# Kernel optimization log

Measured on AMD Instinct MI355X. Metric: run time of the kernel, lower is better.

The kernel has to match this reference:

```python
import jax, jax.numpy as jnp
import numpy as np
import math

B, N, M = 4, 512, 64
F, Q, H, R = 256, 16, 8, 32
D = F // H
ETA = 4.0
EPS = 1e-5
FFN_H = 512

def layer_norm(x, g, b):
    mu = jnp.mean(x, axis=-1, keepdims=True)
    var = jnp.mean((x - mu) ** 2, axis=-1, keepdims=True)
    return (x - mu) * jax.lax.rsqrt(var + EPS) * g + b

def setup_inputs() -> dict:
    key = jax.random.key(0)
    ks = jax.random.split(key, 24)
    def xav(k, shape):
        fan_in, fan_out = shape[1], shape[0]
        std = math.sqrt(2.0 / (fan_in + fan_out))
        return jax.random.normal(k, shape, dtype=jnp.float32) * std
    inp = {
        'a': jax.random.normal(ks[0], (B, N, F), dtype=jnp.float32),
        'charges': jax.random.normal(ks[1], (B, N, Q), dtype=jnp.float32),
        'idx_j': jax.random.randint(ks[2], (B, N, M), 0, N),
        'd_ij': jax.random.uniform(ks[3], (B, N, M), dtype=jnp.float32) * 5.0,
        'mask_ij': jax.random.bernoulli(ks[4], 0.3, (B, N, M)),
        'radial_shifts': jnp.linspace(0.5, 5.0, R, dtype=jnp.float32),
        'Wq': xav(ks[5], (F, F + Q)), 'bq': jnp.zeros((F,), jnp.float32),
        'Wk': xav(ks[6], (F, F + Q)), 'bk': jnp.zeros((F,), jnp.float32),
        'Wv': xav(ks[7], (F, F + Q)), 'bv': jnp.zeros((F,), jnp.float32),
        'Wrb': xav(ks[8], (H, R)), 'brb': jnp.zeros((H,), jnp.float32),
        'Wout': xav(ks[9], (F, 2 * F + R)), 'bout': jnp.zeros((F,), jnp.float32),
        'g1': jnp.ones((F,), jnp.float32), 'b1': jnp.zeros((F,), jnp.float32),
        'g2': jnp.ones((F,), jnp.float32), 'b2': jnp.zeros((F,), jnp.float32),
        'Wf1': xav(ks[10], (FFN_H, F)), 'bf1': jnp.zeros((FFN_H,), jnp.float32),
        'Wf2': xav(ks[11], (F, FFN_H)), 'bf2': jnp.zeros((F,), jnp.float32),
    }
    return inp

def reference(a, charges, idx_j, d_ij, mask_ij, radial_shifts,
              Wq, bq, Wk, bk, Wv, bv, Wrb, brb, Wout, bout,
              g1, b1, g2, b2, Wf1, bf1, Wf2, bf2):
    bidx = jnp.arange(B)[:, None, None]
    a_j = a[bidx, idx_j]          # [B,N,M,F]
    q_j = charges[bidx, idx_j]    # [B,N,M,Q]
    center = jnp.concatenate([a, charges], axis=-1)       # [B,N,F+Q]
    neigh = jnp.concatenate([a_j, q_j], axis=-1)          # [B,N,M,F+Q]
    q = (center @ Wq.T + bq).reshape(B, N, H, D)
    k = (neigh @ Wk.T + bk).reshape(B, N, M, H, D)
    v = (neigh @ Wv.T + bv).reshape(B, N, M, H, D)
    # radial basis: exp(-eta*(d - shift)^2)  -> [B,N,M,R]
    radial = jnp.exp(-ETA * (d_ij[..., None] - radial_shifts) ** 2)
    scores = jnp.einsum('bnhd,bnmhd->bnmh', q, k) / math.sqrt(D)
    scores = scores + radial @ Wrb.T + brb                # [B,N,M,H]
    scores = jnp.swapaxes(scores, -1, -2)                 # [B,N,H,M]
    scores = jnp.where(mask_ij[:, :, None, :], -jnp.inf, scores)
    attn = jax.nn.softmax(scores, axis=-1)
    attn = jnp.nan_to_num(attn, nan=0.0, posinf=0.0, neginf=0.0)
    context = jnp.einsum('bnhm,bnmhd->bnhd', attn, v).reshape(B, N, F)
    radial_context = jnp.einsum('bnhm,bnmg->bnhg', attn, radial).mean(axis=-2)  # [B,N,R]
    update = jnp.concatenate([a, context, radial_context], axis=-1) @ Wout.T + bout
    x = layer_norm(a + update, g1, b1)
    ff = jax.nn.gelu(x @ Wf1.T + bf1, approximate=False) @ Wf2.T + bf2
    return layer_norm(x + ff, g2, b2)
```

## Files before the change

kernel.cpp:

```cpp
#include <hip/hip_runtime.h>
#include <hip/hip_bf16.h>
#include <math.h>

#define Bb 4
#define Nn 512
#define Mm 64
#define Ff 256
#define Qq 16
#define Hh 8
#define Rr 32
#define FFNH 512
#define ROWS (Bb*Nn)
#define KIN (Ff+Qq)
#define KINP 288
#define KOUT (2*Ff+Rr)

typedef short short8 __attribute__((ext_vector_type(8)));
typedef unsigned short ushort8 __attribute__((ext_vector_type(8)));
typedef float f32x4 __attribute__((ext_vector_type(4)));

__device__ inline unsigned short f2b(float f) {
    union { float f; unsigned u; } c; c.f = f;
    unsigned r = c.u + 0x7fffu + ((c.u >> 16) & 1u);
    return (unsigned short)(r >> 16);
}
__device__ inline float b2f(unsigned short u) {
    union { unsigned u; float f; } c; c.u = ((unsigned)u) << 16;
    return c.f;
}

#define OFF_CENTER 0
#define OFF_WQKV   (OFF_CENTER + ROWS*KINP)
#define OFF_WOUT   (OFF_WQKV + 768*KINP)
#define OFF_WF1    (OFF_WOUT + Ff*KOUT)
#define OFF_WF2    (OFF_WF1 + FFNH*Ff)
#define OFF_U      (OFF_WF2 + Ff*FFNH)
#define OFF_XB     (OFF_U + ROWS*KOUT)
#define OFF_FFH    (OFF_XB + ROWS*Ff)
#define OFF_QKVB   (OFF_FFH + ROWS*FFNH)
#define CONV_TOTAL OFF_U
#define CONV_BLK   (CONV_TOTAL/256)
#define A2U_BLK    (ROWS*Ff/256)
#define MSK_BLK    (Bb*Nn*Mm/256)

__global__ __launch_bounds__(256) void prep(const float* __restrict__ a,
                                            const float* __restrict__ ch,
                                            const float* __restrict__ Wq,
                                            const float* __restrict__ Wk,
                                            const float* __restrict__ Wv,
                                            const float* __restrict__ Wout,
                                            const float* __restrict__ Wf1,
                                            const float* __restrict__ Wf2,
                                            const unsigned char* __restrict__ mask,
                                            int* __restrict__ flag,
                                            unsigned short* __restrict__ arena) {
    int bid = blockIdx.x, tid = threadIdx.x;
    if (bid < CONV_BLK) {
        int i = bid * 256 + tid;
        float v;
        if (i < OFF_WQKV) {
            int row = i / KINP, c = i - row * KINP;
            v = (c < Ff) ? a[(size_t)row * Ff + c] : (c < KIN ? ch[(size_t)row * Qq + (c - Ff)] : 0.f);
        } else if (i < OFF_WOUT) {
            int j = i - OFF_WQKV;
            int n = j / KINP, c = j - n * KINP;
            const float* W = n < 256 ? Wq : (n < 512 ? Wk : Wv);
            int nr = n & 255;
            v = (c < KIN) ? W[(size_t)nr * KIN + c] : 0.f;
        } else if (i < OFF_WF1) {
            v = Wout[i - OFF_WOUT];
        } else if (i < OFF_WF2) {
            v = Wf1[i - OFF_WF1];
        } else {
            v = Wf2[i - OFF_WF2];
        }
        arena[i] = f2b(v);
    } else if (bid < CONV_BLK + A2U_BLK) {
        int j = (bid - CONV_BLK) * 256 + tid;
        int row = j >> 8, col = j & 255;
        arena[OFF_U + (size_t)row * KOUT + col] = f2b(a[j]);
    } else {
        int i = (bid - CONV_BLK - A2U_BLK) * 256 + tid;
        if ((i & 3) && mask[i]) *flag = 1;
    }
}

template<int KT, int SPLIT, int MODE>
__global__ __launch_bounds__(256) void gemm_mfma(const unsigned short* __restrict__ Ab, int lda,
                                                 const unsigned short* __restrict__ Wb, int ldw,
                                                 const float* __restrict__ b0,
                                                 const float* __restrict__ b1,
                                                 const float* __restrict__ b2,
                                                 float* __restrict__ C,
                                                 unsigned short* __restrict__ Cb,
                                                 int ldc, size_t pstride) {
    __shared__ unsigned short As[2][64][32];
    __shared__ unsigned short Bs[2][64][32];
    int tid = threadIdx.x;
    int colbase = blockIdx.x * 64;
    int rowbase = blockIdx.y * 64;
    constexpr int TPER = (KT + SPLIT - 1) / SPLIT;
    int t0 = blockIdx.z * TPER;
    int NL = KT - t0; if (NL > TPER) NL = TPER;

    int sr = tid >> 2, sl = tid & 3;
    const unsigned short* Ap = Ab + (size_t)(rowbase + sr) * lda + sl * 8;
    const unsigned short* Wp = Wb + (size_t)(colbase + sr) * ldw + sl * 8;
    int ssw = (sl ^ (sr & 3)) * 8;

    int wave = tid >> 6, lane = tid & 63;
    int wr = (wave >> 1) * 32, wc = (wave & 1) * 32;
    int lrow = lane & 15;
    int kslot = lane >> 4;
    int sp = (kslot ^ (lane & 3)) * 8;

    uint4 av, wv;
    auto prefetch = [&](int t) {
        av = *reinterpret_cast<const uint4*>(Ap + (size_t)t * 32);
        wv = *reinterpret_cast<const uint4*>(Wp + (size_t)t * 32);
    };
    auto writeLDS = [&](int buf) {
        *reinterpret_cast<uint4*>(&As[buf][sr][ssw]) = av;
        *reinterpret_cast<uint4*>(&Bs[buf][sr][ssw]) = wv;
    };

    f32x4 acc[2][2] = {};
    prefetch(t0);
    writeLDS(0);
    __syncthreads();
    for (int tt = 0; tt < NL; ++tt) {
        if (tt + 1 < NL) prefetch(t0 + tt + 1);
        int buf = tt & 1;
        short8 a0 = *reinterpret_cast<const short8*>(&As[buf][wr + lrow][sp]);
        short8 a1 = *reinterpret_cast<const short8*>(&As[buf][wr + 16 + lrow][sp]);
        short8 bv0 = *reinterpret_cast<const short8*>(&Bs[buf][wc + lrow][sp]);
        short8 bv1 = *reinterpret_cast<const short8*>(&Bs[buf][wc + 16 + lrow][sp]);
        acc[0][0] = __builtin_amdgcn_mfma_f32_16x16x32_bf16(a0, bv0, acc[0][0], 0, 0, 0);
        acc[0][1] = __builtin_amdgcn_mfma_f32_16x16x32_bf16(a0, bv1, acc[0][1], 0, 0, 0);
        acc[1][0] = __builtin_amdgcn_mfma_f32_16x16x32_bf16(a1, bv0, acc[1][0], 0, 0, 0);
        acc[1][1] = __builtin_amdgcn_mfma_f32_16x16x32_bf16(a1, bv1, acc[1][1], 0, 0, 0);
        if (tt + 1 < NL) {
            writeLDS((tt + 1) & 1);
            __syncthreads();
        }
    }

    const float* bias = b0;
    if (MODE == 1) {
        int sel = colbase >> 8;
        bias = sel == 0 ? b0 : (sel == 1 ? b1 : b2);
    }
    int colq = (colbase & 255);
    float* Cp = (MODE == 0) ? C + (size_t)blockIdx.z * pstride : C;
    #pragma unroll
    for (int fr = 0; fr < 2; ++fr) {
        #pragma unroll
        for (int fc = 0; fc < 2; ++fc) {
            int coll = wc + fc * 16 + (lane & 15);
            int col = colbase + coll;
            #pragma unroll
            for (int i = 0; i < 4; ++i) {
                int row = rowbase + wr + fr * 16 + (lane >> 4) * 4 + i;
                float v = acc[fr][fc][i];
                if (MODE == 0) {
                    Cp[(size_t)row * ldc + col] = v;
                } else if (MODE == 1) {
                    Cb[(size_t)row * ldc + col] = f2b(v + bias[colq + coll]);
                } else {
                    v += bias[col];
                    v = 0.5f * v * (1.0f + erff(v * 0.70710678118654752f));
                    Cb[(size_t)row * ldc + col] = f2b(v);
                }
            }
        }
    }
}

__global__ __launch_bounds__(256) void attn_kernel(const unsigned short* __restrict__ QKV,
                                                   const int* __restrict__ idx_j,
                                                   const float* __restrict__ d_ij,
                                                   const void* __restrict__ mask,
                                                   const float* __restrict__ shifts,
                                                   const float* __restrict__ Wrb,
                                                   const float* __restrict__ brb,
                                                   const int* __restrict__ flag,
                                                   unsigned short* __restrict__ Ub) {
    __shared__ unsigned short Kt[2][16][280];
    __shared__ float rad[Mm][36];
    __shared__ float att[Hh][Mm];
    __shared__ float attbar[Mm];
    __shared__ int   jl[Mm];
    __shared__ float dv[Mm];
    __shared__ int   maskf[Mm];
    __shared__ float shs[Rr];

    int row = blockIdx.x;
    int b = row >> 9;
    int tid = threadIdx.x;
    bool boolmask = (*flag != 0);

    if (tid < Mm) jl[tid] = idx_j[row * Mm + tid];
    else if (tid < 128) { int m = tid - 64; dv[m] = d_ij[row * Mm + m]; }
    else if (tid < 160) shs[tid - 128] = shifts[tid - 128];
    else if (tid >= 192) {
        int m = tid - 192;
        maskf[m] = boolmask ? (int)((const unsigned char*)mask)[row * Mm + m]
                            : ((const int*)mask)[row * Mm + m];
    }

    int half = tid & 1;
    int p = tid >> 1;
    int hh = p >> 4;
    int ml = p & 15;
    float qf[16];
    {
        const unsigned short* qrow = QKV + (size_t)row * 768 + hh * 32 + half * 16;
        ushort8 q0 = *reinterpret_cast<const ushort8*>(qrow);
        ushort8 q1 = *reinterpret_cast<const ushort8*>(qrow + 8);
        #pragma unroll
        for (int i = 0; i < 8; ++i) { qf[i] = b2f(q0[i]); qf[8 + i] = b2f(q1[i]); }
    }
    float4 wreg[4];
    #pragma unroll
    for (int c = 0; c < 4; ++c)
        wreg[c] = *reinterpret_cast<const float4*>(Wrb + hh * Rr + half * 16 + c * 4);
    float brbh = brb[hh];
    __syncthreads();

    auto stage = [&](int t, int seg, int buf) {
        #pragma unroll
        for (int q = 0; q < 2; ++q) {
            int chunk = q * 256 + tid;
            int r = chunk >> 5, s = chunk & 31;
            int j = jl[t * 16 + r];
            const uint4* src = reinterpret_cast<const uint4*>(QKV + (size_t)(b * Nn + j) * 768 + seg);
            uint4 v = src[s];
            *reinterpret_cast<uint4*>(&Kt[buf][r][s * 8]) = v;
        }
    };

    #pragma unroll
    for (int it = 0; it < 8; ++it) {
        int i = tid + it * 256;
        int m = i >> 5, r = i & 31;
        float t = dv[m] - shs[r];
        rad[m][r] = expf(-4.0f * t * t);
    }
    stage(0, 256, 0);
    __syncthreads();

    for (int t = 0; t < 4; ++t) {
        if (t < 3) stage(t + 1, 256, (t + 1) & 1);
        int buf = t & 1;
        const unsigned short* kr = &Kt[buf][ml][hh * 32 + half * 16];
        ushort8 k0 = *reinterpret_cast<const ushort8*>(kr);
        ushort8 k1 = *reinterpret_cast<const ushort8*>(kr + 8);
        float accK = 0.f;
        #pragma unroll
        for (int i = 0; i < 8; ++i) accK = fmaf(qf[i], b2f(k0[i]), accK);
        #pragma unroll
        for (int i = 0; i < 8; ++i) accK = fmaf(qf[8 + i], b2f(k1[i]), accK);
        float accR = 0.f;
        #pragma unroll
        for (int c = 0; c < 4; ++c) {
            float4 rv = *reinterpret_cast<const float4*>(&rad[t * 16 + ml][half * 16 + c * 4]);
            accR += wreg[c].x * rv.x + wreg[c].y * rv.y + wreg[c].z * rv.z + wreg[c].w * rv.w;
        }
        float tv = accK * 0.17677669529663687f + accR;
        tv += __shfl_xor(tv, 1);
        if (!half) {
            int m = t * 16 + ml;
            att[hh][m] = maskf[m] ? -INFINITY : (tv + brbh);
        }
        __syncthreads();
    }

    {
        int h = tid >> 5, l = tid & 31;
        float s0 = att[h][l], s1 = att[h][l + 32];
        float mx = fmaxf(s0, s1);
        #pragma unroll
        for (int off = 16; off; off >>= 1) mx = fmaxf(mx, __shfl_xor(mx, off, 32));
        float e0 = 0.f, e1 = 0.f;
        if (mx != -INFINITY) {
            e0 = expf(s0 - mx);
            e1 = expf(s1 - mx);
        }
        float sm = e0 + e1;
        #pragma unroll
        for (int off = 16; off; off >>= 1) sm += __shfl_xor(sm, off, 32);
        float inv = sm > 0.f ? 1.f / sm : 0.f;
        att[h][l] = e0 * inv;
        att[h][l + 32] = e1 * inv;
    }
    stage(0, 512, 0);
    __syncthreads();

    float ctx = 0.f;
    int h2 = tid >> 5, d0 = tid & 31;
    for (int t = 0; t < 4; ++t) {
        if (t < 3) stage(t + 1, 512, (t + 1) & 1);
        int buf = t & 1;
        #pragma unroll
        for (int m = 0; m < 16; ++m)
            ctx = fmaf(att[h2][t * 16 + m], b2f(Kt[buf][m][h2 * 32 + d0]), ctx);
        if (t == 0 && tid < Mm) {
            float sv = 0.f;
            #pragma unroll
            for (int h = 0; h < Hh; ++h) sv += att[h][tid];
            attbar[tid] = sv * 0.125f;
        }
        __syncthreads();
    }

    Ub[(size_t)row * KOUT + Ff + tid] = f2b(ctx);

    if (tid < 64) {
        int g = tid >> 1;
        float acc = 0.f;
        #pragma unroll
        for (int i = 0; i < 32; ++i) {
            int m = half * 32 + i;
            acc = fmaf(attbar[m], rad[m][g], acc);
        }
        acc += __shfl_xor(acc, 1);
        if (!half) Ub[(size_t)row * KOUT + 2 * Ff + g] = f2b(acc);
    }
}

template<int S, int WB>
__global__ __launch_bounds__(256) void add_ln_c(const float* __restrict__ x0,
                                                const float* __restrict__ part, size_t pstride,
                                                const float* __restrict__ bias,
                                                const float* __restrict__ g,
                                                const float* __restrict__ be,
                                                float* __restrict__ outp,
                                                unsigned short* __restrict__ xb) {
    int tid = threadIdx.x;
    int wave = tid >> 6, lane = tid & 63;
    int row = blockIdx.x * 4 + wave;
    size_t off = (size_t)row * Ff + lane * 4;
    float4 v = *reinterpret_cast<const float4*>(x0 + off);
    float4 bb = *reinterpret_cast<const float4*>(bias + lane * 4);
    v.x += bb.x; v.y += bb.y; v.z += bb.z; v.w += bb.w;
    #pragma unroll
    for (int s = 0; s < S; ++s) {
        float4 p = *reinterpret_cast<const float4*>(part + (size_t)s * pstride + off);
        v.x += p.x; v.y += p.y; v.z += p.z; v.w += p.w;
    }
    float sm = v.x + v.y + v.z + v.w;
    #pragma unroll
    for (int o = 32; o; o >>= 1) sm += __shfl_xor(sm, o, 64);
    float mu = sm * (1.f / Ff);
    float4 c = {v.x - mu, v.y - mu, v.z - mu, v.w - mu};
    float s2 = c.x * c.x + c.y * c.y + c.z * c.z + c.w * c.w;
    #pragma unroll
    for (int o = 32; o; o >>= 1) s2 += __shfl_xor(s2, o, 64);
    float inv = rsqrtf(s2 * (1.f / Ff) + 1e-5f);
    float4 gg = *reinterpret_cast<const float4*>(g + lane * 4);
    float4 ee = *reinterpret_cast<const float4*>(be + lane * 4);
    float4 r;
    r.x = c.x * inv * gg.x + ee.x;
    r.y = c.y * inv * gg.y + ee.y;
    r.z = c.z * inv * gg.z + ee.z;
    r.w = c.w * inv * gg.w + ee.w;
    *reinterpret_cast<float4*>(outp + off) = r;
    if (WB) {
        ushort4 u;
        u.x = f2b(r.x); u.y = f2b(r.y); u.z = f2b(r.z); u.w = f2b(r.w);
        *reinterpret_cast<ushort4*>(&xb[off]) = u;
    }
}

extern "C" void kernel_launch(void* const* d_in, const int* in_sizes, int n_in,
                              void* d_out, int out_size, void* d_ws, size_t ws_size,
                              hipStream_t stream) {
    const float* a       = (const float*)d_in[0];
    const float* charges = (const float*)d_in[1];
    const int*   idx_j   = (const int*)  d_in[2];
    const float* d_ij    = (const float*)d_in[3];
    const void*  mask    =               d_in[4];
    const float* shifts  = (const float*)d_in[5];
    const float* Wq   = (const float*)d_in[6];  const float* bq   = (const float*)d_in[7];
    const float* Wk   = (const float*)d_in[8];  const float* bk   = (const float*)d_in[9];
    const float* Wv   = (const float*)d_in[10]; const float* bv   = (const float*)d_in[11];
    const float* Wrb  = (const float*)d_in[12]; const float* brb  = (const float*)d_in[13];
    const float* Wout = (const float*)d_in[14]; const float* bout = (const float*)d_in[15];
    const float* g1   = (const float*)d_in[16]; const float* b1   = (const float*)d_in[17];
    const float* g2   = (const float*)d_in[18]; const float* b2   = (const float*)d_in[19];
    const float* Wf1  = (const float*)d_in[20]; const float* bf1  = (const float*)d_in[21];
    const float* Wf2  = (const float*)d_in[22]; const float* bf2  = (const float*)d_in[23];
    float* outp = (float*)d_out;

    float* ws   = (float*)d_ws;
    int*   flag = (int*)d_ws;
    float* part = ws + 1024;
    float* xbuf = part + 1048576;
    unsigned short* arena = (unsigned short*)(xbuf + 524288);
    unsigned short* centerb = arena + OFF_CENTER;
    unsigned short* Wqkvb   = arena + OFF_WQKV;
    unsigned short* Woutb   = arena + OFF_WOUT;
    unsigned short* Wf1b    = arena + OFF_WF1;
    unsigned short* Wf2b    = arena + OFF_WF2;
    unsigned short* Ub      = arena + OFF_U;
    unsigned short* xb      = arena + OFF_XB;
    unsigned short* ffhb    = arena + OFF_FFH;
    unsigned short* QKVB16  = arena + OFF_QKVB;

    hipMemsetAsync(flag, 0, sizeof(int), stream);
    prep<<<CONV_BLK + A2U_BLK + MSK_BLK, 256, 0, stream>>>(
        a, charges, Wq, Wk, Wv, Wout, Wf1, Wf2, (const unsigned char*)mask, flag, arena);

    gemm_mfma<9, 1, 1><<<dim3(12, 32, 1), 256, 0, stream>>>(
        centerb, KINP, Wqkvb, KINP, bq, bk, bv, nullptr, QKVB16, 768, 0);

    attn_kernel<<<ROWS, 256, 0, stream>>>(QKVB16, idx_j, d_ij, mask, shifts, Wrb, brb, flag, Ub);

    gemm_mfma<17, 2, 0><<<dim3(4, 32, 2), 256, 0, stream>>>(
        Ub, KOUT, Woutb, KOUT, nullptr, nullptr, nullptr, part, nullptr, Ff, (size_t)ROWS * Ff);
    add_ln_c<2, 1><<<ROWS / 4, 256, 0, stream>>>(a, part, (size_t)ROWS * Ff, bout, g1, b1, xbuf, xb);

    gemm_mfma<8, 1, 2><<<dim3(8, 32, 1), 256, 0, stream>>>(
        xb, Ff, Wf1b, Ff, bf1, nullptr, nullptr, nullptr, ffhb, FFNH, 0);

    gemm_mfma<16, 2, 0><<<dim3(4, 32, 2), 256, 0, stream>>>(
        ffhb, FFNH, Wf2b, FFNH, nullptr, nullptr, nullptr, part, nullptr, Ff, (size_t)ROWS * Ff);
    add_ln_c<2, 0><<<ROWS / 4, 256, 0, stream>>>(xbuf, part, (size_t)ROWS * Ff, bf2, g2, b2, outp, nullptr);
}
```

Before: 65.64 us.

## Fuse output projection, layernorms and FFN into one row-tiled tail kernel

Replaces the split-K output GEMM, two add+layernorm kernels and two FFN GEMMs with a single kernel. Each block owns 16 rows and keeps the residual, the normalized activations and the GELU hidden layer in LDS, which removes five launches and the fp32 partial-sum and bf16 intermediate round trips through global memory. The QKV GEMM is also rewritten as a 16-row, 512-thread kernel that streams operands straight from global memory into registers, with no LDS staging. Both kernels run only 128 blocks and every block rereads the full weight matrices, so parallelism drops and weight traffic is served from L2.

```diff
diff --git a/kernel.cpp b/kernel.cpp
--- a/kernel.cpp
+++ b/kernel.cpp
@@ -35,9 +35,7 @@
 #define OFF_WF1    (OFF_WOUT + Ff*KOUT)
 #define OFF_WF2    (OFF_WF1 + FFNH*Ff)
 #define OFF_U      (OFF_WF2 + Ff*FFNH)
-#define OFF_XB     (OFF_U + ROWS*KOUT)
-#define OFF_FFH    (OFF_XB + ROWS*Ff)
-#define OFF_QKVB   (OFF_FFH + ROWS*FFNH)
+#define OFF_QKVB   (OFF_U + ROWS*KOUT)
 #define CONV_TOTAL OFF_U
 #define CONV_BLK   (CONV_TOTAL/256)
 #define A2U_BLK    (ROWS*Ff/256)
@@ -85,93 +83,56 @@
     }
 }
 
-template<int KT, int SPLIT, int MODE>
-__global__ __launch_bounds__(256) void gemm_mfma(const unsigned short* __restrict__ Ab, int lda,
-                                                 const unsigned short* __restrict__ Wb, int ldw,
-                                                 const float* __restrict__ b0,
-                                                 const float* __restrict__ b1,
-                                                 const float* __restrict__ b2,
-                                                 float* __restrict__ C,
-                                                 unsigned short* __restrict__ Cb,
-                                                 int ldc, size_t pstride) {
-    __shared__ unsigned short As[2][64][32];
-    __shared__ unsigned short Bs[2][64][32];
+__global__ __launch_bounds__(512) void qkv_gemm(const unsigned short* __restrict__ Ab,
+                                                const unsigned short* __restrict__ Wb,
+                                                const float* __restrict__ bq,
+                                                const float* __restrict__ bk,
+                                                const float* __restrict__ bv,
+                                                unsigned short* __restrict__ QKVb) {
     int tid = threadIdx.x;
-    int colbase = blockIdx.x * 64;
-    int rowbase = blockIdx.y * 64;
-    constexpr int TPER = (KT + SPLIT - 1) / SPLIT;
-    int t0 = blockIdx.z * TPER;
-    int NL = KT - t0; if (NL > TPER) NL = TPER;
-
-    int sr = tid >> 2, sl = tid & 3;
-    const unsigned short* Ap = Ab + (size_t)(rowbase + sr) * lda + sl * 8;
-    const unsigned short* Wp = Wb + (size_t)(colbase + sr) * ldw + sl * 8;
-    int ssw = (sl ^ (sr & 3)) * 8;
-
     int wave = tid >> 6, lane = tid & 63;
-    int wr = (wave >> 1) * 32, wc = (wave & 1) * 32;
-    int lrow = lane & 15;
-    int kslot = lane >> 4;
-    int sp = (kslot ^ (lane & 3)) * 8;
-
-    uint4 av, wv;
-    auto prefetch = [&](int t) {
-        av = *reinterpret_cast<const uint4*>(Ap + (size_t)t * 32);
-        wv = *reinterpret_cast<const uint4*>(Wp + (size_t)t * 32);
-    };
-    auto writeLDS = [&](int buf) {
-        *reinterpret_cast<uint4*>(&As[buf][sr][ssw]) = av;
-        *reinterpret_cast<uint4*>(&Bs[buf][sr][ssw]) = wv;
-    };
-
-    f32x4 acc[2][2] = {};
-    prefetch(t0);
-    writeLDS(0);
-    __syncthreads();
-    for (int tt = 0; tt < NL; ++tt) {
-        if (tt + 1 < NL) prefetch(t0 + tt + 1);
-        int buf = tt & 1;
-        short8 a0 = *reinterpret_cast<const short8*>(&As[buf][wr + lrow][sp]);
-        short8 a1 = *reinterpret_cast<const short8*>(&As[buf][wr + 16 + lrow][sp]);
-        short8 bv0 = *reinterpret_cast<const short8*>(&Bs[buf][wc + lrow][sp]);
-        short8 bv1 = *reinterpret_cast<const short8*>(&Bs[buf][wc + 16 + lrow][sp]);
-        acc[0][0] = __builtin_amdgcn_mfma_f32_16x16x32_bf16(a0, bv0, acc[0][0], 0, 0, 0);
-        acc[0][1] = __builtin_amdgcn_mfma_f32_16x16x32_bf16(a0, bv1, acc[0][1], 0, 0, 0);
-        acc[1][0] = __builtin_amdgcn_mfma_f32_16x16x32_bf16(a1, bv0, acc[1][0], 0, 0, 0);
-        acc[1][1] = __builtin_amdgcn_mfma_f32_16x16x32_bf16(a1, bv1, acc[1][1], 0, 0, 0);
-        if (tt + 1 < NL) {
-            writeLDS((tt + 1) & 1);
-            __syncthreads();
-        }
-    }
-
-    const float* bias = b0;
-    if (MODE == 1) {
-        int sel = colbase >> 8;
-        bias = sel == 0 ? b0 : (sel == 1 ? b1 : b2);
-    }
-    int colq = (colbase & 255);
-    float* Cp = (MODE == 0) ? C + (size_t)blockIdx.z * pstride : C;
+    int rowbase = blockIdx.x * 16;
+    int cb = wave * 96;
+    int lrow = lane & 15, ks = lane >> 4;
+
+    const unsigned short* Ap = Ab + (size_t)(rowbase + lrow) * KINP + ks * 8;
+    const unsigned short* Bp[6];
     #pragma unroll
-    for (int fr = 0; fr < 2; ++fr) {
-        #pragma unroll
-        for (int fc = 0; fc < 2; ++fc) {
-            int coll = wc + fc * 16 + (lane & 15);
-            int col = colbase + coll;
-            #pragma unroll
-            for (int i = 0; i < 4; ++i) {
-                int row = rowbase + wr + fr * 16 + (lane >> 4) * 4 + i;
-                float v = acc[fr][fc][i];
-                if (MODE == 0) {
-                    Cp[(size_t)row * ldc + col] = v;
-                } else if (MODE == 1) {
-                    Cb[(size_t)row * ldc + col] = f2b(v + bias[colq + coll]);
-                } else {
-                    v += bias[col];
-                    v = 0.5f * v * (1.0f + erff(v * 0.70710678118654752f));
-                    Cb[(size_t)row * ldc + col] = f2b(v);
-                }
-            }
+    for (int nt = 0; nt < 6; ++nt)
+        Bp[nt] = Wb + (size_t)(cb + nt * 16 + lrow) * KINP + ks * 8;
+
+    f32x4 acc[6] = {};
+    short8 aC = *reinterpret_cast<const short8*>(Ap);
+    short8 bC[6];
+    #pragma unroll
+    for (int nt = 0; nt < 6; ++nt) bC[nt] = *reinterpret_cast<const short8*>(Bp[nt]);
+    for (int t = 0; t < 8; ++t) {
+        short8 aN = *reinterpret_cast<const short8*>(Ap + (t + 1) * 32);
+        short8 bN[6];
+        #pragma unroll
+        for (int nt = 0; nt < 6; ++nt) bN[nt] = *reinterpret_cast<const short8*>(Bp[nt] + (t + 1) * 32);
+        #pragma unroll
+        for (int nt = 0; nt < 6; ++nt)
+            acc[nt] = __builtin_amdgcn_mfma_f32_16x16x32_bf16(aC, bC[nt], acc[nt], 0, 0, 0);
+        aC = aN;
+        #pragma unroll
+        for (int nt = 0; nt < 6; ++nt) bC[nt] = bN[nt];
+    }
+    #pragma unroll
+    for (int nt = 0; nt < 6; ++nt)
+        acc[nt] = __builtin_amdgcn_mfma_f32_16x16x32_bf16(aC, bC[nt], acc[nt], 0, 0, 0);
+
+    #pragma unroll
+    for (int nt = 0; nt < 6; ++nt) {
+        int col0 = cb + nt * 16;
+        int sel = col0 >> 8;
+        const float* bias = sel == 0 ? bq : (sel == 1 ? bk : bv);
+        int col = col0 + (lane & 15);
+        float badd = bias[(col0 & 255) + (lane & 15)];
+        #pragma unroll
+        for (int i = 0; i < 4; ++i) {
+            int row = rowbase + (lane >> 4) * 4 + i;
+            QKVb[(size_t)row * 768 + col] = f2b(acc[nt][i] + badd);
         }
     }
 }
@@ -328,47 +289,182 @@
     }
 }
 
-template<int S, int WB>
-__global__ __launch_bounds__(256) void add_ln_c(const float* __restrict__ x0,
-                                                const float* __restrict__ part, size_t pstride,
-                                                const float* __restrict__ bias,
-                                                const float* __restrict__ g,
-                                                const float* __restrict__ be,
-                                                float* __restrict__ outp,
-                                                unsigned short* __restrict__ xb) {
+__global__ __launch_bounds__(512) void tail_kernel(const unsigned short* __restrict__ Ub,
+                                                   const unsigned short* __restrict__ Woutb,
+                                                   const unsigned short* __restrict__ Wf1b,
+                                                   const unsigned short* __restrict__ Wf2b,
+                                                   const float* __restrict__ a,
+                                                   const float* __restrict__ bout,
+                                                   const float* __restrict__ g1, const float* __restrict__ b1,
+                                                   const float* __restrict__ bf1,
+                                                   const float* __restrict__ bf2,
+                                                   const float* __restrict__ g2, const float* __restrict__ b2,
+                                                   float* __restrict__ outp) {
+    __shared__ float xs[16][264];
+    __shared__ unsigned short xh[16][264];
+    __shared__ unsigned short hb[16][520];
+
     int tid = threadIdx.x;
     int wave = tid >> 6, lane = tid & 63;
-    int row = blockIdx.x * 4 + wave;
-    size_t off = (size_t)row * Ff + lane * 4;
-    float4 v = *reinterpret_cast<const float4*>(x0 + off);
-    float4 bb = *reinterpret_cast<const float4*>(bias + lane * 4);
-    v.x += bb.x; v.y += bb.y; v.z += bb.z; v.w += bb.w;
-    #pragma unroll
-    for (int s = 0; s < S; ++s) {
-        float4 p = *reinterpret_cast<const float4*>(part + (size_t)s * pstride + off);
-        v.x += p.x; v.y += p.y; v.z += p.z; v.w += p.w;
-    }
-    float sm = v.x + v.y + v.z + v.w;
-    #pragma unroll
-    for (int o = 32; o; o >>= 1) sm += __shfl_xor(sm, o, 64);
-    float mu = sm * (1.f / Ff);
-    float4 c = {v.x - mu, v.y - mu, v.z - mu, v.w - mu};
-    float s2 = c.x * c.x + c.y * c.y + c.z * c.z + c.w * c.w;
-    #pragma unroll
-    for (int o = 32; o; o >>= 1) s2 += __shfl_xor(s2, o, 64);
-    float inv = rsqrtf(s2 * (1.f / Ff) + 1e-5f);
-    float4 gg = *reinterpret_cast<const float4*>(g + lane * 4);
-    float4 ee = *reinterpret_cast<const float4*>(be + lane * 4);
-    float4 r;
-    r.x = c.x * inv * gg.x + ee.x;
-    r.y = c.y * inv * gg.y + ee.y;
-    r.z = c.z * inv * gg.z + ee.z;
-    r.w = c.w * inv * gg.w + ee.w;
-    *reinterpret_cast<float4*>(outp + off) = r;
-    if (WB) {
-        ushort4 u;
-        u.x = f2b(r.x); u.y = f2b(r.y); u.z = f2b(r.z); u.w = f2b(r.w);
-        *reinterpret_cast<ushort4*>(&xb[off]) = u;
+    int rowbase = blockIdx.x * 16;
+    int lrow = lane & 15, ks = lane >> 4;
+
+    {
+        int r = tid >> 5, c = (tid & 31) * 8;
+        float4 a0 = *reinterpret_cast<const float4*>(a + (size_t)(rowbase + r) * Ff + c);
+        float4 a1 = *reinterpret_cast<const float4*>(a + (size_t)(rowbase + r) * Ff + c + 4);
+        float4 o0 = *reinterpret_cast<const float4*>(bout + c);
+        float4 o1 = *reinterpret_cast<const float4*>(bout + c + 4);
+        xs[r][c + 0] = a0.x + o0.x; xs[r][c + 1] = a0.y + o0.y;
+        xs[r][c + 2] = a0.z + o0.z; xs[r][c + 3] = a0.w + o0.w;
+        xs[r][c + 4] = a1.x + o1.x; xs[r][c + 5] = a1.y + o1.y;
+        xs[r][c + 6] = a1.z + o1.z; xs[r][c + 7] = a1.w + o1.w;
+    }
+    __syncthreads();
+
+    {
+        int cb = wave * 32;
+        const unsigned short* Ap = Ub + (size_t)(rowbase + lrow) * KOUT + ks * 8;
+        const unsigned short* B0 = Woutb + (size_t)(cb + lrow) * KOUT + ks * 8;
+        const unsigned short* B1 = Woutb + (size_t)(cb + 16 + lrow) * KOUT + ks * 8;
+        f32x4 acc0 = {}, acc1 = {};
+        short8 aC = *reinterpret_cast<const short8*>(Ap);
+        short8 b0C = *reinterpret_cast<const short8*>(B0);
+        short8 b1C = *reinterpret_cast<const short8*>(B1);
+        for (int t = 0; t < 16; ++t) {
+            short8 aN = *reinterpret_cast<const short8*>(Ap + (t + 1) * 32);
+            short8 b0N = *reinterpret_cast<const short8*>(B0 + (t + 1) * 32);
+            short8 b1N = *reinterpret_cast<const short8*>(B1 + (t + 1) * 32);
+            acc0 = __builtin_amdgcn_mfma_f32_16x16x32_bf16(aC, b0C, acc0, 0, 0, 0);
+            acc1 = __builtin_amdgcn_mfma_f32_16x16x32_bf16(aC, b1C, acc1, 0, 0, 0);
+            aC = aN; b0C = b0N; b1C = b1N;
+        }
+        acc0 = __builtin_amdgcn_mfma_f32_16x16x32_bf16(aC, b0C, acc0, 0, 0, 0);
+        acc1 = __builtin_amdgcn_mfma_f32_16x16x32_bf16(aC, b1C, acc1, 0, 0, 0);
+        #pragma unroll
+        for (int i = 0; i < 4; ++i) {
+            int r = (lane >> 4) * 4 + i;
+            xs[r][cb + (lane & 15)] += acc0[i];
+            xs[r][cb + 16 + (lane & 15)] += acc1[i];
+        }
+    }
+    __syncthreads();
+
+    {
+        int r = wave * 2 + (lane >> 5);
+        int c0 = lane & 31;
+        float v[8]; float sm = 0.f;
+        #pragma unroll
+        for (int j = 0; j < 8; ++j) { v[j] = xs[r][c0 + 32 * j]; sm += v[j]; }
+        #pragma unroll
+        for (int o = 16; o; o >>= 1) sm += __shfl_xor(sm, o);
+        float mu = sm * (1.f / Ff);
+        float s2 = 0.f;
+        #pragma unroll
+        for (int j = 0; j < 8; ++j) { float d = v[j] - mu; s2 += d * d; }
+        #pragma unroll
+        for (int o = 16; o; o >>= 1) s2 += __shfl_xor(s2, o);
+        float inv = rsqrtf(s2 * (1.f / Ff) + 1e-5f);
+        #pragma unroll
+        for (int j = 0; j < 8; ++j) {
+            int c = c0 + 32 * j;
+            float res = (v[j] - mu) * inv * g1[c] + b1[c];
+            xs[r][c] = res;
+            xh[r][c] = f2b(res);
+        }
+    }
+    __syncthreads();
+
+    {
+        int cb = wave * 64;
+        const unsigned short* Bp[4];
+        #pragma unroll
+        for (int nt = 0; nt < 4; ++nt)
+            Bp[nt] = Wf1b + (size_t)(cb + nt * 16 + lrow) * Ff + ks * 8;
+        f32x4 acc[4] = {};
+        short8 bC[4];
+        #pragma unroll
+        for (int nt = 0; nt < 4; ++nt) bC[nt] = *reinterpret_cast<const short8*>(Bp[nt]);
+        for (int t = 0; t < 8; ++t) {
+            short8 bN[4];
+            if (t < 7) {
+                #pragma unroll
+                for (int nt = 0; nt < 4; ++nt) bN[nt] = *reinterpret_cast<const short8*>(Bp[nt] + (t + 1) * 32);
+            }
+            short8 aC = *reinterpret_cast<const short8*>(&xh[lrow][t * 32 + ks * 8]);
+            #pragma unroll
+            for (int nt = 0; nt < 4; ++nt)
+                acc[nt] = __builtin_amdgcn_mfma_f32_16x16x32_bf16(aC, bC[nt], acc[nt], 0, 0, 0);
+            if (t < 7) {
+                #pragma unroll
+                for (int nt = 0; nt < 4; ++nt) bC[nt] = bN[nt];
+            }
+        }
+        #pragma unroll
+        for (int nt = 0; nt < 4; ++nt) {
+            int col = cb + nt * 16 + (lane & 15);
+            float badd = bf1[col];
+            #pragma unroll
+            for (int i = 0; i < 4; ++i) {
+                int r = (lane >> 4) * 4 + i;
+                float v = acc[nt][i] + badd;
+                v = 0.5f * v * (1.0f + erff(v * 0.70710678118654752f));
+                hb[r][col] = f2b(v);
+            }
+        }
+    }
+    __syncthreads();
+
+    {
+        int cb = wave * 32;
+        const unsigned short* B0 = Wf2b + (size_t)(cb + lrow) * FFNH + ks * 8;
+        const unsigned short* B1 = Wf2b + (size_t)(cb + 16 + lrow) * FFNH + ks * 8;
+        f32x4 acc0 = {}, acc1 = {};
+        short8 b0C = *reinterpret_cast<const short8*>(B0);
+        short8 b1C = *reinterpret_cast<const short8*>(B1);
+        for (int t = 0; t < 15; ++t) {
+            short8 b0N = *reinterpret_cast<const short8*>(B0 + (t + 1) * 32);
+            short8 b1N = *reinterpret_cast<const short8*>(B1 + (t + 1) * 32);
+            short8 aC = *reinterpret_cast<const short8*>(&hb[lrow][t * 32 + ks * 8]);
+            acc0 = __builtin_amdgcn_mfma_f32_16x16x32_bf16(aC, b0C, acc0, 0, 0, 0);
+            acc1 = __builtin_amdgcn_mfma_f32_16x16x32_bf16(aC, b1C, acc1, 0, 0, 0);
+            b0C = b0N; b1C = b1N;
+        }
+        {
+            short8 aC = *reinterpret_cast<const short8*>(&hb[lrow][15 * 32 + ks * 8]);
+            acc0 = __builtin_amdgcn_mfma_f32_16x16x32_bf16(aC, b0C, acc0, 0, 0, 0);
+            acc1 = __builtin_amdgcn_mfma_f32_16x16x32_bf16(aC, b1C, acc1, 0, 0, 0);
+        }
+        #pragma unroll
+        for (int i = 0; i < 4; ++i) {
+            int r = (lane >> 4) * 4 + i;
+            int c0 = cb + (lane & 15), c1 = cb + 16 + (lane & 15);
+            xs[r][c0] += acc0[i] + bf2[c0];
+            xs[r][c1] += acc1[i] + bf2[c1];
+        }
+    }
+    __syncthreads();
+
+    {
+        int r = wave * 2 + (lane >> 5);
+        int c0 = lane & 31;
+        float v[8]; float sm = 0.f;
+        #pragma unroll
+        for (int j = 0; j < 8; ++j) { v[j] = xs[r][c0 + 32 * j]; sm += v[j]; }
+        #pragma unroll
+        for (int o = 16; o; o >>= 1) sm += __shfl_xor(sm, o);
+        float mu = sm * (1.f / Ff);
+        float s2 = 0.f;
+        #pragma unroll
+        for (int j = 0; j < 8; ++j) { float d = v[j] - mu; s2 += d * d; }
+        #pragma unroll
+        for (int o = 16; o; o >>= 1) s2 += __shfl_xor(s2, o);
+        float inv = rsqrtf(s2 * (1.f / Ff) + 1e-5f);
+        #pragma unroll
+        for (int j = 0; j < 8; ++j) {
+            int c = c0 + 32 * j;
+            outp[(size_t)(rowbase + r) * Ff + c] = (v[j] - mu) * inv * g2[c] + b2[c];
+        }
     }
 }
 
@@ -394,36 +490,22 @@
 
     float* ws   = (float*)d_ws;
     int*   flag = (int*)d_ws;
-    float* part = ws + 1024;
-    float* xbuf = part + 1048576;
-    unsigned short* arena = (unsigned short*)(xbuf + 524288);
+    unsigned short* arena = (unsigned short*)(ws + 1024);
     unsigned short* centerb = arena + OFF_CENTER;
     unsigned short* Wqkvb   = arena + OFF_WQKV;
     unsigned short* Woutb   = arena + OFF_WOUT;
     unsigned short* Wf1b    = arena + OFF_WF1;
     unsigned short* Wf2b    = arena + OFF_WF2;
     unsigned short* Ub      = arena + OFF_U;
-    unsigned short* xb      = arena + OFF_XB;
-    unsigned short* ffhb    = arena + OFF_FFH;
     unsigned short* QKVB16  = arena + OFF_QKVB;
 
     hipMemsetAsync(flag, 0, sizeof(int), stream);
     prep<<<CONV_BLK + A2U_BLK + MSK_BLK, 256, 0, stream>>>(
         a, charges, Wq, Wk, Wv, Wout, Wf1, Wf2, (const unsigned char*)mask, flag, arena);
 
-    gemm_mfma<9, 1, 1><<<dim3(12, 32, 1), 256, 0, stream>>>(
-        centerb, KINP, Wqkvb, KINP, bq, bk, bv, nullptr, QKVB16, 768, 0);
+    qkv_gemm<<<128, 512, 0, stream>>>(centerb, Wqkvb, bq, bk, bv, QKVB16);
 
     attn_kernel<<<ROWS, 256, 0, stream>>>(QKVB16, idx_j, d_ij, mask, shifts, Wrb, brb, flag, Ub);
 
-    gemm_mfma<17, 2, 0><<<dim3(4, 32, 2), 256, 0, stream>>>(
-        Ub, KOUT, Woutb, KOUT, nullptr, nullptr, nullptr, part, nullptr, Ff, (size_t)ROWS * Ff);
-    add_ln_c<2, 1><<<ROWS / 4, 256, 0, stream>>>(a, part, (size_t)ROWS * Ff, bout, g1, b1, xbuf, xb);
-
-    gemm_mfma<8, 1, 2><<<dim3(8, 32, 1), 256, 0, stream>>>(
-        xb, Ff, Wf1b, Ff, bf1, nullptr, nullptr, nullptr, ffhb, FFNH, 0);
-
-    gemm_mfma<16, 2, 0><<<dim3(4, 32, 2), 256, 0, stream>>>(
-        ffhb, FFNH, Wf2b, FFNH, nullptr, nullptr, nullptr, part, nullptr, Ff, (size_t)ROWS * Ff);
-    add_ln_c<2, 0><<<ROWS / 4, 256, 0, stream>>>(xbuf, part, (size_t)ROWS * Ff, bf2, g2, b2, outp, nullptr);
-}
+    tail_kernel<<<128, 512, 0, stream>>>(Ub, Woutb, Wf1b, Wf2b, a, bout, g1, b1, bf1, bf2, g2, b2, outp);
+}
```

New measurement: 72.42 us. 1.1x slower.

## Fuse first LayerNorm into FFN1 GEMM prologue and vectorise prep kernel

Applied to the files above, without the earlier changes.

The residual add plus LayerNorm after the output projection moves into the prologue of a new FFN1 GEMM kernel. Each block normalises its 64 rows into shared memory as bf16 and then runs the MFMA GEMM with GELU, which removes one launch and the bf16 round trip of x through global memory. The cost is that every column block (8 per row tile) recomputes the same LayerNorm, multiplying that work and the reads of a and part by eight. The prep kernel is also vectorised to handle four elements per thread (sixteen for the mask check), which cuts the block count.

```diff
diff --git a/kernel.cpp b/kernel.cpp
--- a/kernel.cpp
+++ b/kernel.cpp
@@ -39,9 +39,9 @@
 #define OFF_FFH    (OFF_XB + ROWS*Ff)
 #define OFF_QKVB   (OFF_FFH + ROWS*FFNH)
 #define CONV_TOTAL OFF_U
-#define CONV_BLK   (CONV_TOTAL/256)
-#define A2U_BLK    (ROWS*Ff/256)
-#define MSK_BLK    (Bb*Nn*Mm/256)
+#define CONV_BLK4  (CONV_TOTAL/1024)
+#define A2U_BLK4   (ROWS*Ff/1024)
+#define MSK_BLK16  (Bb*Nn*Mm/(256*16))
 
 __global__ __launch_bounds__(256) void prep(const float* __restrict__ a,
                                             const float* __restrict__ ch,
@@ -55,33 +55,41 @@
                                             int* __restrict__ flag,
                                             unsigned short* __restrict__ arena) {
     int bid = blockIdx.x, tid = threadIdx.x;
-    if (bid < CONV_BLK) {
-        int i = bid * 256 + tid;
-        float v;
+    if (bid < CONV_BLK4) {
+        int i = (bid * 256 + tid) * 4;
+        float4 v4 = {0.f, 0.f, 0.f, 0.f};
         if (i < OFF_WQKV) {
             int row = i / KINP, c = i - row * KINP;
-            v = (c < Ff) ? a[(size_t)row * Ff + c] : (c < KIN ? ch[(size_t)row * Qq + (c - Ff)] : 0.f);
+            if (c < Ff)       v4 = *reinterpret_cast<const float4*>(a  + (size_t)row * Ff + c);
+            else if (c < KIN) v4 = *reinterpret_cast<const float4*>(ch + (size_t)row * Qq + (c - Ff));
         } else if (i < OFF_WOUT) {
             int j = i - OFF_WQKV;
             int n = j / KINP, c = j - n * KINP;
             const float* W = n < 256 ? Wq : (n < 512 ? Wk : Wv);
             int nr = n & 255;
-            v = (c < KIN) ? W[(size_t)nr * KIN + c] : 0.f;
+            if (c < KIN) v4 = *reinterpret_cast<const float4*>(W + (size_t)nr * KIN + c);
         } else if (i < OFF_WF1) {
-            v = Wout[i - OFF_WOUT];
+            v4 = *reinterpret_cast<const float4*>(Wout + (i - OFF_WOUT));
         } else if (i < OFF_WF2) {
-            v = Wf1[i - OFF_WF1];
+            v4 = *reinterpret_cast<const float4*>(Wf1 + (i - OFF_WF1));
         } else {
-            v = Wf2[i - OFF_WF2];
-        }
-        arena[i] = f2b(v);
-    } else if (bid < CONV_BLK + A2U_BLK) {
-        int j = (bid - CONV_BLK) * 256 + tid;
+            v4 = *reinterpret_cast<const float4*>(Wf2 + (i - OFF_WF2));
+        }
+        ushort4 u;
+        u.x = f2b(v4.x); u.y = f2b(v4.y); u.z = f2b(v4.z); u.w = f2b(v4.w);
+        *reinterpret_cast<ushort4*>(arena + i) = u;
+    } else if (bid < CONV_BLK4 + A2U_BLK4) {
+        int j = ((bid - CONV_BLK4) * 256 + tid) * 4;
         int row = j >> 8, col = j & 255;
-        arena[OFF_U + (size_t)row * KOUT + col] = f2b(a[j]);
+        float4 v4 = *reinterpret_cast<const float4*>(a + j);
+        ushort4 u;
+        u.x = f2b(v4.x); u.y = f2b(v4.y); u.z = f2b(v4.z); u.w = f2b(v4.w);
+        *reinterpret_cast<ushort4*>(arena + OFF_U + (size_t)row * KOUT + col) = u;
     } else {
-        int i = (bid - CONV_BLK - A2U_BLK) * 256 + tid;
-        if ((i & 3) && mask[i]) *flag = 1;
+        int i = ((bid - CONV_BLK4 - A2U_BLK4) * 256 + tid) * 4;
+        const uint4 v = reinterpret_cast<const uint4*>(mask)[i >> 2];
+        unsigned m = (v.x | v.y | v.z | v.w) & 0xFFFFFF00u;
+        if (m) *flag = 1;
     }
 }
 
@@ -164,12 +172,8 @@
                 float v = acc[fr][fc][i];
                 if (MODE == 0) {
                     Cp[(size_t)row * ldc + col] = v;
-                } else if (MODE == 1) {
+                } else {
                     Cb[(size_t)row * ldc + col] = f2b(v + bias[colq + coll]);
-                } else {
-                    v += bias[col];
-                    v = 0.5f * v * (1.0f + erff(v * 0.70710678118654752f));
-                    Cb[(size_t)row * ldc + col] = f2b(v);
                 }
             }
         }
@@ -328,14 +332,112 @@
     }
 }
 
-template<int S, int WB>
+__global__ __launch_bounds__(256) void ffn1_ln(const float* __restrict__ part, size_t pstride,
+                                               const float* __restrict__ a,
+                                               const float* __restrict__ bout,
+                                               const float* __restrict__ g1,
+                                               const float* __restrict__ b1,
+                                               const unsigned short* __restrict__ Wf1b,
+                                               const float* __restrict__ bf1,
+                                               float* __restrict__ xbuf,
+                                               unsigned short* __restrict__ ffhb) {
+    __shared__ unsigned short Af[64][264];
+    __shared__ unsigned short Bs[2][64][32];
+
+    int tid = threadIdx.x;
+    int wave = tid >> 6, lane = tid & 63;
+    int rowbase = blockIdx.y * 64;
+    int colbase = blockIdx.x * 64;
+
+    int sr = tid >> 2, sl = tid & 3;
+    const unsigned short* Wp = Wf1b + (size_t)(colbase + sr) * Ff + sl * 8;
+    int ssw = (sl ^ (sr & 3)) * 8;
+    uint4 wv = *reinterpret_cast<const uint4*>(Wp);
+
+    {
+        float bo[4], gg[4], bb[4];
+        #pragma unroll
+        for (int j = 0; j < 4; ++j) {
+            int c = lane + 64 * j;
+            bo[j] = bout[c]; gg[j] = g1[c]; bb[j] = b1[c];
+        }
+        for (int rr = 0; rr < 16; ++rr) {
+            int r = wave * 16 + rr;
+            size_t off = (size_t)(rowbase + r) * Ff;
+            float v[4]; float sm = 0.f;
+            #pragma unroll
+            for (int j = 0; j < 4; ++j) {
+                int c = lane + 64 * j;
+                v[j] = a[off + c] + bo[j] + part[off + c] + part[pstride + off + c];
+                sm += v[j];
+            }
+            #pragma unroll
+            for (int o = 32; o; o >>= 1) sm += __shfl_xor(sm, o, 64);
+            float mu = sm * (1.f / Ff);
+            float s2 = 0.f;
+            #pragma unroll
+            for (int j = 0; j < 4; ++j) { float d = v[j] - mu; s2 += d * d; }
+            #pragma unroll
+            for (int o = 32; o; o >>= 1) s2 += __shfl_xor(s2, o, 64);
+            float inv = rsqrtf(s2 * (1.f / Ff) + 1e-5f);
+            #pragma unroll
+            for (int j = 0; j < 4; ++j) {
+                int c = lane + 64 * j;
+                float res = (v[j] - mu) * inv * gg[j] + bb[j];
+                Af[r][c] = f2b(res);
+                if (blockIdx.x == 0) xbuf[off + c] = res;
+            }
+        }
+    }
+    *reinterpret_cast<uint4*>(&Bs[0][sr][ssw]) = wv;
+    __syncthreads();
+
+    int wr = (wave >> 1) * 32, wc = (wave & 1) * 32;
+    int lrow = lane & 15;
+    int kslot = lane >> 4;
+    int sp = (kslot ^ (lane & 3)) * 8;
+
+    f32x4 acc[2][2] = {};
+    for (int tt = 0; tt < 8; ++tt) {
+        if (tt + 1 < 8) wv = *reinterpret_cast<const uint4*>(Wp + (size_t)(tt + 1) * 32);
+        int buf = tt & 1;
+        short8 a0 = *reinterpret_cast<const short8*>(&Af[wr + lrow][tt * 32 + kslot * 8]);
+        short8 a1 = *reinterpret_cast<const short8*>(&Af[wr + 16 + lrow][tt * 32 + kslot * 8]);
+        short8 bv0 = *reinterpret_cast<const short8*>(&Bs[buf][wc + lrow][sp]);
+        short8 bv1 = *reinterpret_cast<const short8*>(&Bs[buf][wc + 16 + lrow][sp]);
+        acc[0][0] = __builtin_amdgcn_mfma_f32_16x16x32_bf16(a0, bv0, acc[0][0], 0, 0, 0);
+        acc[0][1] = __builtin_amdgcn_mfma_f32_16x16x32_bf16(a0, bv1, acc[0][1], 0, 0, 0);
+        acc[1][0] = __builtin_amdgcn_mfma_f32_16x16x32_bf16(a1, bv0, acc[1][0], 0, 0, 0);
+        acc[1][1] = __builtin_amdgcn_mfma_f32_16x16x32_bf16(a1, bv1, acc[1][1], 0, 0, 0);
+        if (tt + 1 < 8) {
+            *reinterpret_cast<uint4*>(&Bs[(tt + 1) & 1][sr][ssw]) = wv;
+            __syncthreads();
+        }
+    }
+
+    #pragma unroll
+    for (int fr = 0; fr < 2; ++fr) {
+        #pragma unroll
+        for (int fc = 0; fc < 2; ++fc) {
+            int col = colbase + wc + fc * 16 + (lane & 15);
+            float badd = bf1[col];
+            #pragma unroll
+            for (int i = 0; i < 4; ++i) {
+                int row = rowbase + wr + fr * 16 + (lane >> 4) * 4 + i;
+                float v = acc[fr][fc][i] + badd;
+                v = 0.5f * v * (1.0f + erff(v * 0.70710678118654752f));
+                ffhb[(size_t)row * FFNH + col] = f2b(v);
+            }
+        }
+    }
+}
+
 __global__ __launch_bounds__(256) void add_ln_c(const float* __restrict__ x0,
                                                 const float* __restrict__ part, size_t pstride,
                                                 const float* __restrict__ bias,
                                                 const float* __restrict__ g,
                                                 const float* __restrict__ be,
-                                                float* __restrict__ outp,
-                                                unsigned short* __restrict__ xb) {
+                                                float* __restrict__ outp) {
     int tid = threadIdx.x;
     int wave = tid >> 6, lane = tid & 63;
     int row = blockIdx.x * 4 + wave;
@@ -344,7 +446,7 @@
     float4 bb = *reinterpret_cast<const float4*>(bias + lane * 4);
     v.x += bb.x; v.y += bb.y; v.z += bb.z; v.w += bb.w;
     #pragma unroll
-    for (int s = 0; s < S; ++s) {
+    for (int s = 0; s < 2; ++s) {
         float4 p = *reinterpret_cast<const float4*>(part + (size_t)s * pstride + off);
         v.x += p.x; v.y += p.y; v.z += p.z; v.w += p.w;
     }
@@ -365,11 +467,6 @@
     r.z = c.z * inv * gg.z + ee.z;
     r.w = c.w * inv * gg.w + ee.w;
     *reinterpret_cast<float4*>(outp + off) = r;
-    if (WB) {
-        ushort4 u;
-        u.x = f2b(r.x); u.y = f2b(r.y); u.z = f2b(r.z); u.w = f2b(r.w);
-        *reinterpret_cast<ushort4*>(&xb[off]) = u;
-    }
 }
 
 extern "C" void kernel_launch(void* const* d_in, const int* in_sizes, int n_in,
@@ -403,12 +500,11 @@
     unsigned short* Wf1b    = arena + OFF_WF1;
     unsigned short* Wf2b    = arena + OFF_WF2;
     unsigned short* Ub      = arena + OFF_U;
-    unsigned short* xb      = arena + OFF_XB;
     unsigned short* ffhb    = arena + OFF_FFH;
     unsigned short* QKVB16  = arena + OFF_QKVB;
 
     hipMemsetAsync(flag, 0, sizeof(int), stream);
-    prep<<<CONV_BLK + A2U_BLK + MSK_BLK, 256, 0, stream>>>(
+    prep<<<CONV_BLK4 + A2U_BLK4 + MSK_BLK16, 256, 0, stream>>>(
         a, charges, Wq, Wk, Wv, Wout, Wf1, Wf2, (const unsigned char*)mask, flag, arena);
 
     gemm_mfma<9, 1, 1><<<dim3(12, 32, 1), 256, 0, stream>>>(
@@ -418,12 +514,11 @@
 
     gemm_mfma<17, 2, 0><<<dim3(4, 32, 2), 256, 0, stream>>>(
         Ub, KOUT, Woutb, KOUT, nullptr, nullptr, nullptr, part, nullptr, Ff, (size_t)ROWS * Ff);
-    add_ln_c<2, 1><<<ROWS / 4, 256, 0, stream>>>(a, part, (size_t)ROWS * Ff, bout, g1, b1, xbuf, xb);
-
-    gemm_mfma<8, 1, 2><<<dim3(8, 32, 1), 256, 0, stream>>>(
-        xb, Ff, Wf1b, Ff, bf1, nullptr, nullptr, nullptr, ffhb, FFNH, 0);
+
+    ffn1_ln<<<dim3(8, 32), 256, 0, stream>>>(
+        part, (size_t)ROWS * Ff, a, bout, g1, b1, Wf1b, bf1, xbuf, ffhb);
 
     gemm_mfma<16, 2, 0><<<dim3(4, 32, 2), 256, 0, stream>>>(
         ffhb, FFNH, Wf2b, FFNH, nullptr, nullptr, nullptr, part, nullptr, Ff, (size_t)ROWS * Ff);
-    add_ln_c<2, 0><<<ROWS / 4, 256, 0, stream>>>(xbuf, part, (size_t)ROWS * Ff, bf2, g2, b2, outp, nullptr);
-}
+    add_ln_c<<<ROWS / 4, 256, 0, stream>>>(xbuf, part, (size_t)ROWS * Ff, bf2, g2, b2, outp);
+}
```

Result: slower. 75.66 us (+15.3%).
